# Performance work log

Hardware: AMD Instinct MI355X
Metric: run time of the kernel (lower is better)

Reference implementation:

```python
import jax, jax.numpy as jnp
import numpy as np

EPS = 1e-12  # matches torch F.normalize eps


def _l2_normalize(x, axis):
    n = jnp.linalg.norm(x, axis=axis, keepdims=True)
    return x / jnp.maximum(n, EPS)


def setup_inputs() -> dict:
    key = jax.random.key(0)
    k1, k2 = jax.random.split(key)
    B, C, h, w = 16, 64, 21, 21
    n_classes, M = 10, 2205  # M = shot(5) * h*w(441)
    x1 = jax.random.normal(k1, (B, C, h, w), dtype=jnp.float32)
    x2 = jax.random.normal(k2, (n_classes, C, M), dtype=jnp.float32)
    return {"x1": x1, "x2": x2, "neighbor_k": 3}


def reference(x1, x2, neighbor_k):
    B, C, h, w = x1.shape
    # queries: [B, h*w, C] local descriptors, L2-normalized per descriptor
    q = _l2_normalize(x1.reshape(B, C, h * w).transpose(0, 2, 1), axis=-1)
    # support: [n, C, M], normalized along channel dim (torch dim=0 per class)
    s = _l2_normalize(x2, axis=1)
    # all pairwise cosine similarities: [B, n, h*w, M]
    inner = jnp.einsum('bqc,ncm->bnqm', q, s)
    topv, _ = jax.lax.top_k(inner, neighbor_k)  # [B, n, h*w, k]
    return topv.sum(axis=(2, 3))  # [B, n]
```

## Files before the change

### kernel.cpp

```cpp
#include <hip/hip_runtime.h>
#include <math.h>

#define BB    16
#define CC    64
#define HW    441
#define QP    448
#define NCLS  10
#define MM    2205
#define MP    2208
#define CHUNK_T 6
#define CHUNK_BYTES (CHUNK_T * 16 * CC * 2)

typedef _Float16 half8 __attribute__((ext_vector_type(8)));
typedef float   float4_ __attribute__((ext_vector_type(4)));

#define WAIT_VMCNT(n) __builtin_amdgcn_s_waitcnt(0x0F70 | (n))

#define GLDS16(g, l) __builtin_amdgcn_global_load_lds(                         \
    (const __attribute__((address_space(1))) unsigned int*)(const void*)(g),   \
    (__attribute__((address_space(3))) unsigned int*)(void*)(l), 16, 0, 0)

__device__ __forceinline__ void ins3(float d, float& a0, float& a1, float& a2) {
    float n0 = fmaxf(d, a0);
    float n1 = __builtin_amdgcn_fmed3f(d, a0, a1);
    float n2 = __builtin_amdgcn_fmed3f(d, a1, a2);
    a0 = n0; a1 = n1; a2 = n2;
}

__global__ __launch_bounds__(256) void prep(const float* __restrict__ x1,
                                            const float* __restrict__ x2,
                                            _Float16* __restrict__ qn,
                                            _Float16* __restrict__ sn) {
    __shared__ float ssred[256];
    __shared__ half8 obuf[256];
    int tid = threadIdx.x;
    int ml = tid & 31, cg = tid >> 5;
    float v[8];
    half8* dstblk;
    int wz;
    if (blockIdx.x < BB * 14) {
        int b = blockIdx.x / 14, pt = blockIdx.x % 14;
        int p = pt * 32 + ml;
        const float* src = x1 + (size_t)b * CC * HW + p;
        bool real = p < HW;
        #pragma unroll
        for (int i = 0; i < 8; ++i) v[i] = real ? src[(size_t)(cg * 8 + i) * HW] : 0.f;
        wz = cg;
        dstblk = (half8*)(qn + ((size_t)(b * QP + pt * 32)) * CC);
    } else {
        int sb = blockIdx.x - BB * 14;
        int n = sb / 69, mt = sb % 69;
        int m = mt * 32 + ml;
        const float* src = x2 + (size_t)n * CC * MM + m;
        bool real = m < MM;
        #pragma unroll
        for (int i = 0; i < 8; ++i) v[i] = real ? src[(size_t)(cg * 8 + i) * MM] : 0.f;
        wz = cg ^ (ml & 7);
        dstblk = (half8*)(sn + ((size_t)(n * MP + mt * 32)) * CC);
    }
    float ss = 0.f;
    #pragma unroll
    for (int i = 0; i < 8; ++i) ss += v[i] * v[i];
    ssred[tid] = ss;
    __syncthreads();
    float tot = 0.f;
    #pragma unroll
    for (int j = 0; j < 8; ++j) tot += ssred[j * 32 + ml];
    float inv = 1.f / fmaxf(sqrtf(tot), 1e-12f);
    half8 h;
    #pragma unroll
    for (int i = 0; i < 8; ++i) h[i] = (_Float16)(v[i] * inv);
    obuf[ml * 8 + wz] = h;
    __syncthreads();
    dstblk[tid] = obuf[tid];
}

__global__ __launch_bounds__(256) void img2class_mfma(const _Float16* __restrict__ qn,
                                                      const _Float16* __restrict__ sn,
                                                      float* __restrict__ partial) {
    __shared__ half8 ldsv[2 * CHUNK_T * 16 * 8];
    _Float16* lds = (_Float16*)ldsv;

    int mh = blockIdx.x & 1;
    int t  = blockIdx.x >> 1;
    int bn = t / 7, qg = t % 7;
    int b = bn / NCLS, n = bn % NCLS;
    int nch    = mh ? 11 : 12;
    int mtile0 = mh ? 72 : 0;

    int tid  = threadIdx.x;
    int wave = tid >> 6, lane = tid & 63;
    int col  = lane & 15, quad = lane >> 4;
    int q0 = (qg * 4 + wave) * 16;

    const half8* Ap = (const half8*)(qn + ((size_t)(b * QP + q0 + col)) * CC + quad * 8);
    half8 A0 = Ap[0];
    half8 A1 = Ap[4];

    float t0[4], t1[4], t2[4];
    #pragma unroll
    for (int r = 0; r < 4; ++r) { t0[r] = -1.0e30f; t1[r] = -1.0e30f; t2[r] = -1.0e30f; }

    float pen = (col >= 13) ? -1.0e30f : 0.0f;

    const char* sbase = (const char*)(sn + (size_t)n * MP * CC) + (size_t)mtile0 * 16 * CC * 2;
    int so = (wave * 3) * 1024 + lane * 16;
    char* lbase = (char*)lds;

    #pragma unroll
    for (int i = 0; i < 3; ++i)
        GLDS16(sbase + so + i * 1024, lbase + (wave * 3 + i) * 1024);

    int sw0 = ((0 ^ (col & 7)) << 3) + col * CC;
    (void)sw0;

    for (int chunk = 0; chunk < nch; ++chunk) {
        if (chunk + 1 < nch) {
            const char* g = sbase + (size_t)(chunk + 1) * CHUNK_BYTES + so;
            char* l = lbase + ((chunk + 1) & 1) * CHUNK_BYTES + (wave * 3) * 1024;
            #pragma unroll
            for (int i = 0; i < 3; ++i)
                GLDS16(g + i * 1024, l + i * 1024);
            WAIT_VMCNT(3);
        } else {
            WAIT_VMCNT(0);
        }
        __builtin_amdgcn_s_barrier();

        const _Float16* lb = lds + (chunk & 1) * (CHUNK_T * 16 * CC);
        bool lastc = (mh == 1) && (chunk == nch - 1);
        #pragma unroll
        for (int pr = 0; pr < 3; ++pr) {
            int re = (pr * 2) * 16 + col;
            int ro = (pr * 2 + 1) * 16 + col;
            half8 B0e = *(const half8*)(lb + re * CC + ((quad       ^ (col & 7)) << 3));
            half8 B1e = *(const half8*)(lb + re * CC + (((4 + quad) ^ (col & 7)) << 3));
            half8 B0o = *(const half8*)(lb + ro * CC + ((quad       ^ (col & 7)) << 3));
            half8 B1o = *(const half8*)(lb + ro * CC + (((4 + quad) ^ (col & 7)) << 3));
            float4_ z = {0.f, 0.f, 0.f, 0.f};
            float4_ ae = __builtin_amdgcn_mfma_f32_16x16x32_f16(A0, B0e, z, 0, 0, 0);
            ae = __builtin_amdgcn_mfma_f32_16x16x32_f16(A1, B1e, ae, 0, 0, 0);
            float4_ ao = __builtin_amdgcn_mfma_f32_16x16x32_f16(A0, B0o, z, 0, 0, 0);
            ao = __builtin_amdgcn_mfma_f32_16x16x32_f16(A1, B1o, ao, 0, 0, 0);
            if (lastc && pr == 2) { ao.x += pen; ao.y += pen; ao.z += pen; ao.w += pen; }
            float d0 = fmaxf(ae.x, ao.x);
            float d1 = fmaxf(ae.y, ao.y);
            float d2 = fmaxf(ae.z, ao.z);
            float d3 = fmaxf(ae.w, ao.w);
            ins3(d0, t0[0], t1[0], t2[0]);
            ins3(d1, t0[1], t1[1], t2[1]);
            ins3(d2, t0[2], t1[2], t2[2]);
            ins3(d3, t0[3], t1[3], t2[3]);
        }
        __syncthreads();
    }

    #pragma unroll
    for (int step = 1; step <= 8; step <<= 1) {
        #pragma unroll
        for (int r = 0; r < 4; ++r) {
            float o0 = __shfl_xor(t0[r], step);
            float o1 = __shfl_xor(t1[r], step);
            float o2 = __shfl_xor(t2[r], step);
            ins3(o0, t0[r], t1[r], t2[r]);
            ins3(o1, t0[r], t1[r], t2[r]);
            ins3(o2, t0[r], t1[r], t2[r]);
        }
    }

    if (col == 0) {
        float* pp = partial + ((size_t)((bn * 7 + qg) * 2 + mh) * 64 + wave * 16 + quad * 4) * 3;
        #pragma unroll
        for (int r = 0; r < 4; ++r) {
            pp[r * 3 + 0] = t0[r];
            pp[r * 3 + 1] = t1[r];
            pp[r * 3 + 2] = t2[r];
        }
    }
}

__global__ __launch_bounds__(512) void merge_halves(const float* __restrict__ partial,
                                                    float* __restrict__ out) {
    __shared__ float red[512];
    int bn = blockIdx.x;
    int q  = threadIdx.x;
    float s = 0.f;
    if (q < HW) {
        int qg = q >> 6, ql = q & 63;
        const float* p0 = partial + ((size_t)((bn * 7 + qg) * 2 + 0) * 64 + ql) * 3;
        const float* p1 = partial + ((size_t)((bn * 7 + qg) * 2 + 1) * 64 + ql) * 3;
        float a0 = p0[0], a1 = p0[1], a2 = p0[2];
        ins3(p1[0], a0, a1, a2);
        ins3(p1[1], a0, a1, a2);
        ins3(p1[2], a0, a1, a2);
        s = a0 + a1 + a2;
    }
    red[q] = s;
    __syncthreads();
    #pragma unroll
    for (int stride = 256; stride >= 1; stride >>= 1) {
        if (q < stride) red[q] += red[q + stride];
        __syncthreads();
    }
    if (q == 0) out[bn] = red[0];
}

extern "C" void kernel_launch(void* const* d_in, const int* in_sizes, int n_in,
                              void* d_out, int out_size, void* d_ws, size_t ws_size,
                              hipStream_t stream) {
    const float* x1 = (const float*)d_in[0];
    const float* x2 = (const float*)d_in[1];
    float* out = (float*)d_out;

    _Float16* qn   = (_Float16*)d_ws;
    _Float16* sn   = qn + (size_t)BB * QP * CC;
    float* partial = (float*)(sn + (size_t)NCLS * MP * CC);

    prep<<<BB * 14 + NCLS * 69, 256, 0, stream>>>(x1, x2, qn, sn);
    img2class_mfma<<<BB * NCLS * 7 * 2, 256, 0, stream>>>(qn, sn, partial);
    merge_halves<<<BB * NCLS, 512, 0, stream>>>(partial, out);
}
```

Measured before the change: 106.6 us.

## Hold query tiles in registers, give each wave its own support tiles, fuse merge

Each block now covers the full support set for 112 queries. The seven query tiles sit in registers, and each wave streams its own 32-row slice of the support chunks through a private double buffer in LDS. This removes the block-wide barrier inside the loop and reuses each LDS support fragment across seven query tiles. The separate merge kernel and the partial buffer are gone: top-3 lists are reduced across waves in LDS and the per-block sum is added to the output atomically, with a memset to zero the output first. The trade-off is fewer blocks (640 instead of 2240), more registers per thread, and a non-deterministic float summation order from the atomics.

```diff
diff --git a/kernel.cpp b/kernel.cpp
--- a/kernel.cpp
+++ b/kernel.cpp
@@ -7,9 +7,12 @@
 #define QP    448
 #define NCLS  10
 #define MM    2205
-#define MP    2208
-#define CHUNK_T 6
-#define CHUNK_BYTES (CHUNK_T * 16 * CC * 2)
+#define MP2   2304
+#define CH_T  8
+#define CH_B  (CH_T * 16 * CC * 2)
+#define NCH   18
+#define NQT   7
+#define NQG   4
 
 typedef _Float16 half8 __attribute__((ext_vector_type(8)));
 typedef float   float4_ __attribute__((ext_vector_type(4)));
@@ -49,14 +52,14 @@
         dstblk = (half8*)(qn + ((size_t)(b * QP + pt * 32)) * CC);
     } else {
         int sb = blockIdx.x - BB * 14;
-        int n = sb / 69, mt = sb % 69;
+        int n = sb / 72, mt = sb % 72;
         int m = mt * 32 + ml;
         const float* src = x2 + (size_t)n * CC * MM + m;
         bool real = m < MM;
         #pragma unroll
         for (int i = 0; i < 8; ++i) v[i] = real ? src[(size_t)(cg * 8 + i) * MM] : 0.f;
         wz = cg ^ (ml & 7);
-        dstblk = (half8*)(sn + ((size_t)(n * MP + mt * 32)) * CC);
+        dstblk = (half8*)(sn + ((size_t)(n * MP2 + mt * 32)) * CC);
     }
     float ss = 0.f;
     #pragma unroll
@@ -75,134 +78,145 @@
     dstblk[tid] = obuf[tid];
 }
 
-__global__ __launch_bounds__(256) void img2class_mfma(const _Float16* __restrict__ qn,
-                                                      const _Float16* __restrict__ sn,
-                                                      float* __restrict__ partial) {
-    __shared__ half8 ldsv[2 * CHUNK_T * 16 * 8];
-    _Float16* lds = (_Float16*)ldsv;
-
-    int mh = blockIdx.x & 1;
-    int t  = blockIdx.x >> 1;
-    int bn = t / 7, qg = t % 7;
+__global__ __launch_bounds__(256, 3) void img2class_mfma(const _Float16* __restrict__ qn,
+                                                         const _Float16* __restrict__ sn,
+                                                         float* __restrict__ out) {
+    __shared__ half8 ldsv[2 * CH_T * 16 * 8];
+    _Float16* ldsh = (_Float16*)ldsv;
+    char* lbase = (char*)ldsv;
+
+    int t  = blockIdx.x;
+    int bn = t / NQG, qg = t % NQG;
     int b = bn / NCLS, n = bn % NCLS;
-    int nch    = mh ? 11 : 12;
-    int mtile0 = mh ? 72 : 0;
 
     int tid  = threadIdx.x;
     int wave = tid >> 6, lane = tid & 63;
     int col  = lane & 15, quad = lane >> 4;
-    int q0 = (qg * 4 + wave) * 16;
-
-    const half8* Ap = (const half8*)(qn + ((size_t)(b * QP + q0 + col)) * CC + quad * 8);
-    half8 A0 = Ap[0];
-    half8 A1 = Ap[4];
-
-    float t0[4], t1[4], t2[4];
-    #pragma unroll
-    for (int r = 0; r < 4; ++r) { t0[r] = -1.0e30f; t1[r] = -1.0e30f; t2[r] = -1.0e30f; }
-
-    float pen = (col >= 13) ? -1.0e30f : 0.0f;
-
-    const char* sbase = (const char*)(sn + (size_t)n * MP * CC) + (size_t)mtile0 * 16 * CC * 2;
-    int so = (wave * 3) * 1024 + lane * 16;
-    char* lbase = (char*)lds;
-
-    #pragma unroll
-    for (int i = 0; i < 3; ++i)
-        GLDS16(sbase + so + i * 1024, lbase + (wave * 3 + i) * 1024);
-
-    int sw0 = ((0 ^ (col & 7)) << 3) + col * CC;
-    (void)sw0;
-
-    for (int chunk = 0; chunk < nch; ++chunk) {
-        if (chunk + 1 < nch) {
-            const char* g = sbase + (size_t)(chunk + 1) * CHUNK_BYTES + so;
-            char* l = lbase + ((chunk + 1) & 1) * CHUNK_BYTES + (wave * 3) * 1024;
+    int q0 = qg * (NQT * 16);
+
+    const char* sbase = (const char*)(sn + (size_t)n * MP2 * CC);
+    int so   = wave * 4096 + lane * 16;
+    int ldst = wave * 4096;
+
+    #pragma unroll
+    for (int i = 0; i < 4; ++i)
+        GLDS16(sbase + so + i * 1024, lbase + ldst + i * 1024);
+
+    const half8* Qp = (const half8*)(qn + ((size_t)(b * QP + q0 + col)) * CC) + quad;
+    half8 Q0[NQT], Q1[NQT];
+    #pragma unroll
+    for (int qt = 0; qt < NQT; ++qt) {
+        Q0[qt] = Qp[qt * 128];
+        Q1[qt] = Qp[qt * 128 + 4];
+    }
+
+    float T0[NQT], T1[NQT], T2[NQT];
+    #pragma unroll
+    for (int qt = 0; qt < NQT; ++qt) { T0[qt] = -1.0e30f; T1[qt] = -1.0e30f; T2[qt] = -1.0e30f; }
+
+    int offE0 = col * CC + ((quad       ^ (col & 7)) << 3);
+    int offE1 = col * CC + (((4 + quad) ^ (col & 7)) << 3);
+
+    for (int c = 0; c < NCH; ++c) {
+        if (c + 1 < NCH) {
+            __builtin_amdgcn_sched_barrier(0);
+            const char* g = sbase + (size_t)(c + 1) * CH_B + so;
+            char* l = lbase + ((c + 1) & 1) * CH_B + ldst;
             #pragma unroll
-            for (int i = 0; i < 3; ++i)
+            for (int i = 0; i < 4; ++i)
                 GLDS16(g + i * 1024, l + i * 1024);
-            WAIT_VMCNT(3);
+            WAIT_VMCNT(4);
         } else {
             WAIT_VMCNT(0);
         }
-        __builtin_amdgcn_s_barrier();
-
-        const _Float16* lb = lds + (chunk & 1) * (CHUNK_T * 16 * CC);
-        bool lastc = (mh == 1) && (chunk == nch - 1);
-        #pragma unroll
-        for (int pr = 0; pr < 3; ++pr) {
-            int re = (pr * 2) * 16 + col;
-            int ro = (pr * 2 + 1) * 16 + col;
-            half8 B0e = *(const half8*)(lb + re * CC + ((quad       ^ (col & 7)) << 3));
-            half8 B1e = *(const half8*)(lb + re * CC + (((4 + quad) ^ (col & 7)) << 3));
-            half8 B0o = *(const half8*)(lb + ro * CC + ((quad       ^ (col & 7)) << 3));
-            half8 B1o = *(const half8*)(lb + ro * CC + (((4 + quad) ^ (col & 7)) << 3));
-            float4_ z = {0.f, 0.f, 0.f, 0.f};
-            float4_ ae = __builtin_amdgcn_mfma_f32_16x16x32_f16(A0, B0e, z, 0, 0, 0);
-            ae = __builtin_amdgcn_mfma_f32_16x16x32_f16(A1, B1e, ae, 0, 0, 0);
-            float4_ ao = __builtin_amdgcn_mfma_f32_16x16x32_f16(A0, B0o, z, 0, 0, 0);
-            ao = __builtin_amdgcn_mfma_f32_16x16x32_f16(A1, B1o, ao, 0, 0, 0);
-            if (lastc && pr == 2) { ao.x += pen; ao.y += pen; ao.z += pen; ao.w += pen; }
+        __builtin_amdgcn_sched_barrier(0);
+
+        const _Float16* lw = ldsh + (c & 1) * (CH_T * 16 * CC) + wave * (32 * CC);
+        half8 S0e = *(const half8*)(lw + offE0);
+        half8 S1e = *(const half8*)(lw + offE1);
+        half8 S0o = *(const half8*)(lw + offE0 + 16 * CC);
+        half8 S1o = *(const half8*)(lw + offE1 + 16 * CC);
+
+        int tE = c * CH_T + wave * 2;
+        bool dopen = (tE >= 136);
+        float pE0 = 0.f, pE1 = 0.f, pE2 = 0.f, pE3 = 0.f;
+        float pO0 = 0.f, pO1 = 0.f, pO2 = 0.f, pO3 = 0.f;
+        if (dopen) {
+            int mE = tE * 16 + quad * 4;
+            pE0 = (mE +  0 >= MM) ? -1.0e30f : 0.f;
+            pE1 = (mE +  1 >= MM) ? -1.0e30f : 0.f;
+            pE2 = (mE +  2 >= MM) ? -1.0e30f : 0.f;
+            pE3 = (mE +  3 >= MM) ? -1.0e30f : 0.f;
+            pO0 = (mE + 16 >= MM) ? -1.0e30f : 0.f;
+            pO1 = (mE + 17 >= MM) ? -1.0e30f : 0.f;
+            pO2 = (mE + 18 >= MM) ? -1.0e30f : 0.f;
+            pO3 = (mE + 19 >= MM) ? -1.0e30f : 0.f;
+        }
+
+        float4_ z = {0.f, 0.f, 0.f, 0.f};
+        #pragma unroll
+        for (int qt = 0; qt < NQT; ++qt) {
+            float4_ ae = __builtin_amdgcn_mfma_f32_16x16x32_f16(S0e, Q0[qt], z, 0, 0, 0);
+            ae = __builtin_amdgcn_mfma_f32_16x16x32_f16(S1e, Q1[qt], ae, 0, 0, 0);
+            float4_ ao = __builtin_amdgcn_mfma_f32_16x16x32_f16(S0o, Q0[qt], z, 0, 0, 0);
+            ao = __builtin_amdgcn_mfma_f32_16x16x32_f16(S1o, Q1[qt], ao, 0, 0, 0);
+            if (dopen) {
+                ae.x += pE0; ae.y += pE1; ae.z += pE2; ae.w += pE3;
+                ao.x += pO0; ao.y += pO1; ao.z += pO2; ao.w += pO3;
+            }
             float d0 = fmaxf(ae.x, ao.x);
             float d1 = fmaxf(ae.y, ao.y);
             float d2 = fmaxf(ae.z, ao.z);
             float d3 = fmaxf(ae.w, ao.w);
-            ins3(d0, t0[0], t1[0], t2[0]);
-            ins3(d1, t0[1], t1[1], t2[1]);
-            ins3(d2, t0[2], t1[2], t2[2]);
-            ins3(d3, t0[3], t1[3], t2[3]);
-        }
-        __syncthreads();
-    }
-
-    #pragma unroll
-    for (int step = 1; step <= 8; step <<= 1) {
-        #pragma unroll
-        for (int r = 0; r < 4; ++r) {
-            float o0 = __shfl_xor(t0[r], step);
-            float o1 = __shfl_xor(t1[r], step);
-            float o2 = __shfl_xor(t2[r], step);
-            ins3(o0, t0[r], t1[r], t2[r]);
-            ins3(o1, t0[r], t1[r], t2[r]);
-            ins3(o2, t0[r], t1[r], t2[r]);
-        }
-    }
-
-    if (col == 0) {
-        float* pp = partial + ((size_t)((bn * 7 + qg) * 2 + mh) * 64 + wave * 16 + quad * 4) * 3;
-        #pragma unroll
-        for (int r = 0; r < 4; ++r) {
-            pp[r * 3 + 0] = t0[r];
-            pp[r * 3 + 1] = t1[r];
-            pp[r * 3 + 2] = t2[r];
-        }
-    }
-}
-
-__global__ __launch_bounds__(512) void merge_halves(const float* __restrict__ partial,
-                                                    float* __restrict__ out) {
-    __shared__ float red[512];
-    int bn = blockIdx.x;
-    int q  = threadIdx.x;
+            ins3(d0, T0[qt], T1[qt], T2[qt]);
+            ins3(d1, T0[qt], T1[qt], T2[qt]);
+            ins3(d2, T0[qt], T1[qt], T2[qt]);
+            ins3(d3, T0[qt], T1[qt], T2[qt]);
+        }
+    }
+
+    #pragma unroll
+    for (int step = 16; step <= 32; step <<= 1) {
+        #pragma unroll
+        for (int qt = 0; qt < NQT; ++qt) {
+            float o0 = __shfl_xor(T0[qt], step);
+            float o1 = __shfl_xor(T1[qt], step);
+            float o2 = __shfl_xor(T2[qt], step);
+            ins3(o0, T0[qt], T1[qt], T2[qt]);
+            ins3(o1, T0[qt], T1[qt], T2[qt]);
+            ins3(o2, T0[qt], T1[qt], T2[qt]);
+        }
+    }
+
+    float* dumpW = (float*)(lbase + wave * 4096);
+    if (quad == 0) {
+        #pragma unroll
+        for (int qt = 0; qt < NQT; ++qt) {
+            float* dp = dumpW + (qt * 16 + col) * 3;
+            dp[0] = T0[qt]; dp[1] = T1[qt]; dp[2] = T2[qt];
+        }
+    }
+    __syncthreads();
+
     float s = 0.f;
-    if (q < HW) {
-        int qg = q >> 6, ql = q & 63;
-        const float* p0 = partial + ((size_t)((bn * 7 + qg) * 2 + 0) * 64 + ql) * 3;
-        const float* p1 = partial + ((size_t)((bn * 7 + qg) * 2 + 1) * 64 + ql) * 3;
-        float a0 = p0[0], a1 = p0[1], a2 = p0[2];
-        ins3(p1[0], a0, a1, a2);
-        ins3(p1[1], a0, a1, a2);
-        ins3(p1[2], a0, a1, a2);
+    if (tid < NQT * 16) {
+        const float* d0 = (const float*)(lbase) + tid * 3;
+        float a0 = d0[0], a1 = d0[1], a2 = d0[2];
+        #pragma unroll
+        for (int w = 1; w < 4; ++w) {
+            const float* dw = (const float*)(lbase + w * 4096) + tid * 3;
+            ins3(dw[0], a0, a1, a2);
+            ins3(dw[1], a0, a1, a2);
+            ins3(dw[2], a0, a1, a2);
+        }
         s = a0 + a1 + a2;
     }
-    red[q] = s;
-    __syncthreads();
-    #pragma unroll
-    for (int stride = 256; stride >= 1; stride >>= 1) {
-        if (q < stride) red[q] += red[q + stride];
-        __syncthreads();
-    }
-    if (q == 0) out[bn] = red[0];
+    #pragma unroll
+    for (int step = 1; step < 64; step <<= 1) s += __shfl_xor(s, step);
+    float* wsum = (float*)(lbase + CH_B);
+    if (lane == 0) wsum[wave] = s;
+    __syncthreads();
+    if (tid == 0) atomicAdd(&out[bn], wsum[0] + wsum[1] + wsum[2] + wsum[3]);
 }
 
 extern "C" void kernel_launch(void* const* d_in, const int* in_sizes, int n_in,
@@ -212,11 +226,10 @@
     const float* x2 = (const float*)d_in[1];
     float* out = (float*)d_out;
 
-    _Float16* qn   = (_Float16*)d_ws;
-    _Float16* sn   = qn + (size_t)BB * QP * CC;
-    float* partial = (float*)(sn + (size_t)NCLS * MP * CC);
-
-    prep<<<BB * 14 + NCLS * 69, 256, 0, stream>>>(x1, x2, qn, sn);
-    img2class_mfma<<<BB * NCLS * 7 * 2, 256, 0, stream>>>(qn, sn, partial);
-    merge_halves<<<BB * NCLS, 512, 0, stream>>>(partial, out);
-}
+    _Float16* qn = (_Float16*)d_ws;
+    _Float16* sn = qn + (size_t)BB * QP * CC;
+
+    hipMemsetAsync(d_out, 0, out_size, stream);
+    prep<<<BB * 14 + NCLS * 72, 256, 0, stream>>>(x1, x2, qn, sn);
+    img2class_mfma<<<BB * NCLS * NQG, 256, 0, stream>>>(qn, sn, out);
+}
```

New measurement: 108.6 us. About the same (+1.8%).
